# Performance work log

Hardware: AMD Instinct MI355X
Metric: run time of the kernel (lower is better)

## Reference

```python
import jax, jax.numpy as jnp
import numpy as np

N = 10000   # nodes
E = 320000  # edges
G = 64      # graphs in batch
D = 256     # gnn embedding dim
A = 118     # atomic_num_dim
OUT = 100   # spectrum dim
NUM_GINE = 2


def setup_inputs() -> dict:
    key = jax.random.key(0)
    ks = jax.random.split(key, 16)
    inp = {
        'atomic_num': jax.random.normal(ks[0], (N, A), dtype=jnp.float32),
        'length': jax.random.uniform(ks[1], (E,), dtype=jnp.float32),
        'src': jax.random.randint(ks[2], (E,), 0, N, dtype=jnp.int32),
        'dst': jax.random.randint(ks[3], (E,), 0, N, dtype=jnp.int32),
        'graph_ids': jnp.sort(jax.random.randint(ks[4], (N,), 0, G, dtype=jnp.int32)),
        # parameters
        'W_node': jax.random.normal(ks[5], (A, D), dtype=jnp.float32) / np.sqrt(A),
        'b_node': jnp.zeros((D,), dtype=jnp.float32),
        'W_edge': jax.random.normal(ks[6], (1, D), dtype=jnp.float32),
        'b_edge': jnp.zeros((D,), dtype=jnp.float32),
        'gine_eps': jnp.zeros((NUM_GINE,), dtype=jnp.float32),  # learnable eps per GINEConv
        'W_gnn': jax.random.normal(ks[7], (NUM_GINE, D, D), dtype=jnp.float32) / np.sqrt(D),
        'b_gnn': jnp.zeros((NUM_GINE, D), dtype=jnp.float32),
        'eps_param': jnp.array([1e-3], dtype=jnp.float32),  # unify_vector eps
        'W_mlp': jax.random.normal(ks[8], (D, OUT), dtype=jnp.float32) / np.sqrt(D),
        'b_mlp': jnp.zeros((OUT,), dtype=jnp.float32),
    }
    return inp


def reference(atomic_num, length, src, dst, graph_ids,
              W_node, b_node, W_edge, b_edge,
              gine_eps, W_gnn, b_gnn, eps_param, W_mlp, b_mlp):
    # node / edge embeddings
    h = atomic_num @ W_node + b_node            # [N, D]
    e = length[:, None] @ W_edge + b_edge       # [E, D]
    # GINEConv layers: m_ij = relu(h_src + e_ij); h_i' = W((1+eps)h_i + sum_j m_ij) + b
    for i in range(NUM_GINE):
        m = jax.nn.relu(h[src] + e)             # [E, D] gather + elementwise
        agg = jax.ops.segment_sum(m, dst, num_segments=N)  # scatter-sum to dst nodes
        h = ((1.0 + gine_eps[i]) * h + agg) @ W_gnn[i] + b_gnn[i]
    # sum_nodes pooling per graph
    feat = jax.ops.segment_sum(h, graph_ids, num_segments=G)  # [G, D]
    # unify_vector: global min/max normalization
    mn = jnp.min(feat)
    mx = jnp.max(feat)
    feat = (feat - mn) / (eps_param[0] + mx - mn)
    # MLP head (no hidden layers): Linear(D, 100)
    return feat @ W_mlp + b_mlp                 # [G, 100]
```

## Files before the change

kernel.cpp:

```cpp
#include <hip/hip_runtime.h>
#include <hip/hip_bf16.h>

#define N_NODES 10000
#define N_EDGES 320000
#define N_GRAPHS 64
#define DIM 256
#define ADIM 118
#define OUTD 100
#define CAP 96
#define CURPAD 16

typedef short bf8_t __attribute__((ext_vector_type(8)));
typedef float f4_t  __attribute__((ext_vector_type(4)));

__device__ __forceinline__ unsigned short f2bf(float f) {
    unsigned u = __float_as_uint(f);
    u += 0x7FFFu + ((u >> 16) & 1u);
    return (unsigned short)(u >> 16);
}
__device__ __forceinline__ float bf2f(unsigned short s) {
    return __uint_as_float(((unsigned)s) << 16);
}

__global__ __launch_bounds__(256) void convW_k(
    const float* __restrict__ Wn, const float* __restrict__ Wg,
    unsigned short* __restrict__ WnT, unsigned short* __restrict__ WgT,
    int* __restrict__ cursor, float* __restrict__ feat) {
    int i = blockIdx.x * 256 + threadIdx.x;
    if (i < 32768) {
        int c = i >> 7, k = i & 127;
        WnT[i] = (k < ADIM) ? f2bf(Wn[k * DIM + c]) : (unsigned short)0;
    } else {
        int j = i - 32768;
        int l = j >> 16, rem = j & 65535;
        int c = rem >> 8, k = rem & 255;
        WgT[j] = f2bf(Wg[l * 65536 + k * DIM + c]);
    }
    if (i < N_NODES * CURPAD) cursor[i] = (i >> 4) * CAP;
    if (i < N_GRAPHS * DIM) feat[i] = 0.f;
}

__global__ __launch_bounds__(256) void fill_k(
    const int* __restrict__ src, const int* __restrict__ dst,
    const float* __restrict__ len, int* __restrict__ cursor,
    int2* __restrict__ epack) {
    int j = blockIdx.x * 256 + threadIdx.x;
    if (j >= N_EDGES) return;
    int d = dst[j];
    int pos = atomicAdd(&cursor[d << 4], 1);
    if (pos < d * CAP + CAP)
        epack[pos] = make_int2(src[j], __float_as_int(len[j]));
}

#define AST 136
__global__ __launch_bounds__(256) void node_embed_k(
    const float* __restrict__ an, const unsigned short* __restrict__ WnT,
    const float* __restrict__ bn, unsigned short* __restrict__ hbf) {
    __shared__ __attribute__((aligned(16))) unsigned short xs[16 * AST];
    const int base = blockIdx.x * 16;
    const int tid = threadIdx.x;
    for (int i = tid; i < 16 * (AST - ADIM); i += 256) {
        int r = i / (AST - ADIM);
        int c = i - r * (AST - ADIM);
        xs[r * AST + ADIM + c] = 0;
    }
    for (int i = tid; i < 16 * 59; i += 256) {
        int r = i / 59;
        int c = (i - r * 59) * 2;
        float2 v = *(const float2*)(an + (size_t)(base + r) * ADIM + c);
        xs[r * AST + c]     = f2bf(v.x);
        xs[r * AST + c + 1] = f2bf(v.y);
    }
    __syncthreads();
    const int wave = tid >> 6, lane = tid & 63;
    const int m = lane & 15, quad = lane >> 4;
    bf8_t afrag[4];
    #pragma unroll
    for (int s = 0; s < 4; ++s)
        afrag[s] = *(const bf8_t*)&xs[m * AST + s * 32 + quad * 8];
    const int colbase = wave * 64;
    #pragma unroll
    for (int ct = 0; ct < 4; ++ct) {
        f4_t acc = (f4_t){0.f, 0.f, 0.f, 0.f};
        const unsigned short* wp = WnT + (size_t)(colbase + ct * 16 + m) * 128 + quad * 8;
        #pragma unroll
        for (int s = 0; s < 4; ++s) {
            bf8_t bfrag = *(const bf8_t*)(wp + s * 32);
            acc = __builtin_amdgcn_mfma_f32_16x16x32_bf16(afrag[s], bfrag, acc, 0, 0, 0);
        }
        int col = colbase + ct * 16 + m;
        float bb = bn[col];
        #pragma unroll
        for (int r = 0; r < 4; ++r)
            hbf[(size_t)(base + quad * 4 + r) * DIM + col] = f2bf(acc[r] + bb);
    }
}

__global__ __launch_bounds__(256) void gather_k(
    const unsigned short* __restrict__ hbf, const int* __restrict__ cursor,
    const int2* __restrict__ epack, const float* __restrict__ We,
    const float* __restrict__ be, const float* __restrict__ epsp, int layer,
    unsigned short* __restrict__ xbf) {
    const int B = blockIdx.x;
    const int half = (B >> 2) & 1;
    const int k = (B >> 3) * 4 + (B & 3);
    const int wave = threadIdx.x >> 6, lane = threadIdx.x & 63;
    const int node = __builtin_amdgcn_readfirstlane(k * 4 + wave);
    const int sub = lane >> 4;
    const int dp = half * 128 + (lane & 15) * 8;
    float4 wa = *(const float4*)(We + dp);
    float4 wc = *(const float4*)(We + dp + 4);
    float4 b0 = *(const float4*)(be + dp);
    float4 b1 = *(const float4*)(be + dp + 4);
    float w[8]  = {wa.x, wa.y, wa.z, wa.w, wc.x, wc.y, wc.z, wc.w};
    float bv[8] = {b0.x, b0.y, b0.z, b0.w, b1.x, b1.y, b1.z, b1.w};
    float acc[8];
    #pragma unroll
    for (int i = 0; i < 8; ++i) acc[i] = 0.f;
    const unsigned short* hb = hbf + dp;
    const int lo = node * CAP;
    const int cnt = min(__builtin_amdgcn_readfirstlane(cursor[node * CURPAD]) - lo, CAP);
    const int2* ep = epack + lo;
#define GATH(q) { \
    bf8_t a = *(const bf8_t*)(hb + (size_t)(q).x * DIM); \
    float l = __int_as_float((q).y); \
    _Pragma("unroll") \
    for (int d = 0; d < 8; ++d) \
        acc[d] += fmaxf(bf2f((unsigned short)a[d]) + fmaf(l, w[d], bv[d]), 0.f); }
    int t = 0;
    for (; t + 7 < cnt; t += 8) {
        int2 qa = ep[t + sub], qb = ep[t + 4 + sub];
        GATH(qa) GATH(qb)
    }
    for (; t + 3 < cnt; t += 4) {
        int2 q = ep[t + sub];
        GATH(q)
    }
    if (t < cnt && t + sub < cnt) {
        int2 q = ep[t + sub];
        GATH(q)
    }
#undef GATH
    #pragma unroll
    for (int d = 0; d < 8; ++d) {
        acc[d] += __shfl(acc[d], lane ^ 16, 64);
        acc[d] += __shfl(acc[d], lane ^ 32, 64);
    }
    if (sub == 0) {
        const float eps1 = 1.f + epsp[layer];
        bf8_t hv = *(const bf8_t*)(hbf + (size_t)node * DIM + dp);
        bf8_t o;
        #pragma unroll
        for (int d = 0; d < 8; ++d)
            o[d] = (short)f2bf(fmaf(eps1, bf2f((unsigned short)hv[d]), acc[d]));
        *(bf8_t*)(xbf + (size_t)node * DIM + dp) = o;
    }
}

#define XST 264
__global__ __launch_bounds__(256) void update_k(
    const unsigned short* __restrict__ xbf,
    const unsigned short* __restrict__ WT, const float* __restrict__ b,
    unsigned short* __restrict__ hout,
    const int* __restrict__ gid, float* __restrict__ feat, int do_pool) {
    __shared__ __attribute__((aligned(16))) unsigned short xs[16 * XST];
    __shared__ int gids[16];
    const int rb = blockIdx.x >> 1;
    const int halfc = blockIdx.x & 1;
    const int base = rb * 16;
    const int tid = threadIdx.x;
    #pragma unroll
    for (int cch = tid; cch < 512; cch += 256) {
        int rr = cch >> 5, k0 = (cch & 31) * 8;
        *(bf8_t*)&xs[rr * XST + k0] = *(const bf8_t*)(xbf + (size_t)(base + rr) * DIM + k0);
    }
    if (do_pool && tid < 16) gids[tid] = gid[base + tid];
    __syncthreads();
    const int wave = tid >> 6, lane = tid & 63;
    const int m = lane & 15, quad = lane >> 4;
    bf8_t afrag[8];
    #pragma unroll
    for (int s = 0; s < 8; ++s)
        afrag[s] = *(const bf8_t*)&xs[m * XST + s * 32 + quad * 8];
    const int colbase = halfc * 128 + wave * 32;
    #pragma unroll
    for (int ct = 0; ct < 2; ++ct) {
        const int col = colbase + ct * 16 + m;
        f4_t acc2 = (f4_t){0.f, 0.f, 0.f, 0.f};
        const unsigned short* wp = WT + (size_t)col * DIM + quad * 8;
        #pragma unroll
        for (int s = 0; s < 8; ++s) {
            bf8_t bfrag = *(const bf8_t*)(wp + s * 32);
            acc2 = __builtin_amdgcn_mfma_f32_16x16x32_bf16(afrag[s], bfrag, acc2, 0, 0, 0);
        }
        const float bb = b[col];
        if (!do_pool) {
            #pragma unroll
            for (int r = 0; r < 4; ++r)
                hout[(size_t)(base + quad * 4 + r) * DIM + col] = f2bf(acc2[r] + bb);
        } else {
            if (gids[0] == gids[15]) {
                float v = acc2[0] + acc2[1] + acc2[2] + acc2[3] + 4.f * bb;
                v += __shfl(v, lane ^ 16, 64);
                v += __shfl(v, lane ^ 32, 64);
                if (quad == 0) atomicAdd(&feat[(size_t)gids[0] * DIM + col], v);
            } else {
                float run = 0.f;
                int cur = gids[quad * 4];
                #pragma unroll
                for (int r = 0; r < 4; ++r) {
                    int g = gids[quad * 4 + r];
                    if (g != cur) {
                        atomicAdd(&feat[(size_t)cur * DIM + col], run);
                        run = 0.f;
                        cur = g;
                    }
                    run += acc2[r] + bb;
                }
                atomicAdd(&feat[(size_t)cur * DIM + col], run);
            }
        }
    }
}

__global__ __launch_bounds__(256) void headmm_k(
    const float* __restrict__ feat, const float* __restrict__ Wm,
    const float* __restrict__ bm, const float* __restrict__ epsp,
    float* __restrict__ out) {
    __shared__ float frow[DIM];
    __shared__ float smn[4], smx[4], sMn, sMx;
    const int g = blockIdx.x;
    const int tid = threadIdx.x;
    float mn = 3.4e38f, mx = -3.4e38f;
    for (int i = tid; i < N_GRAPHS * DIM; i += 256) {
        float v = feat[i];
        mn = fminf(mn, v);
        mx = fmaxf(mx, v);
    }
    frow[tid] = feat[g * DIM + tid];
    #pragma unroll
    for (int off = 32; off > 0; off >>= 1) {
        mn = fminf(mn, __shfl_down(mn, off, 64));
        mx = fmaxf(mx, __shfl_down(mx, off, 64));
    }
    const int wave = tid >> 6, lane = tid & 63;
    if (lane == 0) { smn[wave] = mn; smx[wave] = mx; }
    __syncthreads();
    if (tid == 0) {
        sMn = fminf(fminf(smn[0], smn[1]), fminf(smn[2], smn[3]));
        sMx = fmaxf(fmaxf(smx[0], smx[1]), fmaxf(smx[2], smx[3]));
    }
    __syncthreads();
    if (tid < OUTD) {
        const float mnv = sMn;
        const float inv = 1.f / (epsp[0] + sMx - mnv);
        float acc = 0.f;
        for (int d = 0; d < DIM; ++d)
            acc += (frow[d] - mnv) * Wm[d * OUTD + tid];
        out[g * OUTD + tid] = acc * inv + bm[tid];
    }
}

extern "C" void kernel_launch(void* const* d_in, const int* in_sizes, int n_in,
                              void* d_out, int out_size, void* d_ws, size_t ws_size,
                              hipStream_t stream) {
    const float* atomic_num = (const float*)d_in[0];
    const float* length     = (const float*)d_in[1];
    const int*   src        = (const int*)d_in[2];
    const int*   dst        = (const int*)d_in[3];
    const int*   gid        = (const int*)d_in[4];
    const float* W_node     = (const float*)d_in[5];
    const float* b_node     = (const float*)d_in[6];
    const float* W_edge     = (const float*)d_in[7];
    const float* b_edge     = (const float*)d_in[8];
    const float* gine_eps   = (const float*)d_in[9];
    const float* W_gnn      = (const float*)d_in[10];
    const float* b_gnn      = (const float*)d_in[11];
    const float* eps_param  = (const float*)d_in[12];
    const float* W_mlp      = (const float*)d_in[13];
    const float* b_mlp      = (const float*)d_in[14];
    float* out = (float*)d_out;

    float* feat = (float*)d_ws;
    int* cursor = (int*)(feat + (size_t)N_GRAPHS * DIM);
    int2* epack = (int2*)(cursor + (size_t)N_NODES * CURPAD + 16);
    unsigned short* hbf0 = (unsigned short*)(epack + (size_t)N_NODES * CAP);
    unsigned short* hbf1 = hbf0 + (size_t)N_NODES * DIM;
    unsigned short* xbf  = hbf1 + (size_t)N_NODES * DIM;
    unsigned short* WnT  = xbf + (size_t)N_NODES * DIM;
    unsigned short* WgT  = WnT + 256 * 128;

    convW_k<<<640, 256, 0, stream>>>(W_node, W_gnn, WnT, WgT, cursor, feat);
    fill_k<<<N_EDGES / 256, 256, 0, stream>>>(src, dst, length, cursor, epack);
    node_embed_k<<<N_NODES / 16, 256, 0, stream>>>(atomic_num, WnT, b_node, hbf0);

    gather_k<<<5000, 256, 0, stream>>>(
        hbf0, cursor, epack, W_edge, b_edge, gine_eps, 0, xbf);
    update_k<<<(N_NODES / 16) * 2, 256, 0, stream>>>(
        xbf, WgT, b_gnn, hbf1, gid, feat, 0);
    gather_k<<<5000, 256, 0, stream>>>(
        hbf1, cursor, epack, W_edge, b_edge, gine_eps, 1, xbf);
    update_k<<<(N_NODES / 16) * 2, 256, 0, stream>>>(
        xbf, WgT + 256 * 256, b_gnn + DIM, hbf0, gid, feat, 1);

    headmm_k<<<N_GRAPHS, 256, 0, stream>>>(feat, W_mlp, b_mlp, eps_param, out);
}
```

Measured before the change: 205.5 us.

## Fold edge bias into node features, use packed FMA in gather, merge setup kernels

```diff
diff --git a/kernel.cpp b/kernel.cpp
--- a/kernel.cpp
+++ b/kernel.cpp
@@ -12,6 +12,7 @@
 
 typedef short bf8_t __attribute__((ext_vector_type(8)));
 typedef float f4_t  __attribute__((ext_vector_type(4)));
+typedef float f2_t  __attribute__((ext_vector_type(2)));
 
 __device__ __forceinline__ unsigned short f2bf(float f) {
     unsigned u = __float_as_uint(f);
@@ -21,41 +22,50 @@
 __device__ __forceinline__ float bf2f(unsigned short s) {
     return __uint_as_float(((unsigned)s) << 16);
 }
-
-__global__ __launch_bounds__(256) void convW_k(
+__device__ __forceinline__ f2_t pk_fma(f2_t a, f2_t b, f2_t c) {
+    f2_t d;
+    asm("v_pk_fma_f32 %0, %1, %2, %3" : "=v"(d) : "v"(a), "v"(b), "v"(c));
+    return d;
+}
+__device__ __forceinline__ f2_t pk_add(f2_t a, f2_t b) {
+    f2_t d;
+    asm("v_pk_add_f32 %0, %1, %2" : "=v"(d) : "v"(a), "v"(b));
+    return d;
+}
+
+__global__ __launch_bounds__(256) void setup_k(
+    const int* __restrict__ src, const int* __restrict__ dst,
+    const float* __restrict__ len,
     const float* __restrict__ Wn, const float* __restrict__ Wg,
     unsigned short* __restrict__ WnT, unsigned short* __restrict__ WgT,
-    int* __restrict__ cursor, float* __restrict__ feat) {
-    int i = blockIdx.x * 256 + threadIdx.x;
-    if (i < 32768) {
-        int c = i >> 7, k = i & 127;
-        WnT[i] = (k < ADIM) ? f2bf(Wn[k * DIM + c]) : (unsigned short)0;
+    int* __restrict__ cnt, int2* __restrict__ epack) {
+    const int B = blockIdx.x;
+    const int tid = threadIdx.x;
+    if (B < 1250) {
+        int j = B * 256 + tid;
+        int d = dst[j];
+        int pos = atomicAdd(&cnt[d << 4], 1);
+        if (pos < CAP)
+            epack[d * CAP + pos] = make_int2(src[j] * DIM, __float_as_int(len[j]));
     } else {
-        int j = i - 32768;
-        int l = j >> 16, rem = j & 65535;
-        int c = rem >> 8, k = rem & 255;
-        WgT[j] = f2bf(Wg[l * 65536 + k * DIM + c]);
-    }
-    if (i < N_NODES * CURPAD) cursor[i] = (i >> 4) * CAP;
-    if (i < N_GRAPHS * DIM) feat[i] = 0.f;
-}
-
-__global__ __launch_bounds__(256) void fill_k(
-    const int* __restrict__ src, const int* __restrict__ dst,
-    const float* __restrict__ len, int* __restrict__ cursor,
-    int2* __restrict__ epack) {
-    int j = blockIdx.x * 256 + threadIdx.x;
-    if (j >= N_EDGES) return;
-    int d = dst[j];
-    int pos = atomicAdd(&cursor[d << 4], 1);
-    if (pos < d * CAP + CAP)
-        epack[pos] = make_int2(src[j], __float_as_int(len[j]));
+        int i = (B - 1250) * 256 + tid;
+        if (i < 32768) {
+            int c = i >> 7, k = i & 127;
+            WnT[i] = (k < ADIM) ? f2bf(Wn[k * DIM + c]) : (unsigned short)0;
+        } else {
+            int j = i - 32768;
+            int l = j >> 16, rem = j & 65535;
+            int c = rem >> 8, k = rem & 255;
+            WgT[j] = f2bf(Wg[l * 65536 + k * DIM + c]);
+        }
+    }
 }
 
 #define AST 136
 __global__ __launch_bounds__(256) void node_embed_k(
     const float* __restrict__ an, const unsigned short* __restrict__ WnT,
-    const float* __restrict__ bn, unsigned short* __restrict__ hbf) {
+    const float* __restrict__ bn, const float* __restrict__ be,
+    unsigned short* __restrict__ hbf) {
     __shared__ __attribute__((aligned(16))) unsigned short xs[16 * AST];
     const int base = blockIdx.x * 16;
     const int tid = threadIdx.x;
@@ -89,7 +99,7 @@
             acc = __builtin_amdgcn_mfma_f32_16x16x32_bf16(afrag[s], bfrag, acc, 0, 0, 0);
         }
         int col = colbase + ct * 16 + m;
-        float bb = bn[col];
+        float bb = bn[col] + be[col];
         #pragma unroll
         for (int r = 0; r < 4; ++r)
             hbf[(size_t)(base + quad * 4 + r) * DIM + col] = f2bf(acc[r] + bb);
@@ -97,7 +107,7 @@
 }
 
 __global__ __launch_bounds__(256) void gather_k(
-    const unsigned short* __restrict__ hbf, const int* __restrict__ cursor,
+    const unsigned short* __restrict__ hbf, const int* __restrict__ cnt,
     const int2* __restrict__ epack, const float* __restrict__ We,
     const float* __restrict__ be, const float* __restrict__ epsp, int layer,
     unsigned short* __restrict__ xbf) {
@@ -110,49 +120,70 @@
     const int dp = half * 128 + (lane & 15) * 8;
     float4 wa = *(const float4*)(We + dp);
     float4 wc = *(const float4*)(We + dp + 4);
-    float4 b0 = *(const float4*)(be + dp);
-    float4 b1 = *(const float4*)(be + dp + 4);
-    float w[8]  = {wa.x, wa.y, wa.z, wa.w, wc.x, wc.y, wc.z, wc.w};
-    float bv[8] = {b0.x, b0.y, b0.z, b0.w, b1.x, b1.y, b1.z, b1.w};
-    float acc[8];
-    #pragma unroll
-    for (int i = 0; i < 8; ++i) acc[i] = 0.f;
+    f2_t ww[4];
+    ww[0] = (f2_t){wa.x, wa.y}; ww[1] = (f2_t){wa.z, wa.w};
+    ww[2] = (f2_t){wc.x, wc.y}; ww[3] = (f2_t){wc.z, wc.w};
+    const float eps1 = 1.f + epsp[layer];
+    float4 ba = *(const float4*)(be + dp);
+    float4 bc = *(const float4*)(be + dp + 4);
+    f2_t ebe[4];
+    ebe[0] = (f2_t){eps1 * ba.x, eps1 * ba.y};
+    ebe[1] = (f2_t){eps1 * ba.z, eps1 * ba.w};
+    ebe[2] = (f2_t){eps1 * bc.x, eps1 * bc.y};
+    ebe[3] = (f2_t){eps1 * bc.z, eps1 * bc.w};
+    f2_t acc2[4];
+    #pragma unroll
+    for (int i = 0; i < 4; ++i) acc2[i] = (f2_t){0.f, 0.f};
     const unsigned short* hb = hbf + dp;
-    const int lo = node * CAP;
-    const int cnt = min(__builtin_amdgcn_readfirstlane(cursor[node * CURPAD]) - lo, CAP);
-    const int2* ep = epack + lo;
+    const int ce = min(__builtin_amdgcn_readfirstlane(cnt[node << 4]), CAP);
+    const int2* ep = epack + node * CAP;
 #define GATH(q) { \
-    bf8_t a = *(const bf8_t*)(hb + (size_t)(q).x * DIM); \
-    float l = __int_as_float((q).y); \
+    const uint4 ar = *(const uint4*)(hb + (unsigned)(q).x); \
+    const float l = __int_as_float((q).y); \
+    f2_t lpk; lpk.x = l; lpk.y = l; \
     _Pragma("unroll") \
-    for (int d = 0; d < 8; ++d) \
-        acc[d] += fmaxf(bf2f((unsigned short)a[d]) + fmaf(l, w[d], bv[d]), 0.f); }
+    for (int p = 0; p < 4; ++p) { \
+        unsigned u = (&ar.x)[p]; \
+        f2_t h; \
+        h.x = __uint_as_float(u << 16); \
+        h.y = __uint_as_float(u & 0xffff0000u); \
+        f2_t mm = pk_fma(lpk, ww[p], h); \
+        mm.x = fmaxf(mm.x, 0.f); \
+        mm.y = fmaxf(mm.y, 0.f); \
+        acc2[p] = pk_add(acc2[p], mm); \
+    } }
     int t = 0;
-    for (; t + 7 < cnt; t += 8) {
+    for (; t + 7 < ce; t += 8) {
         int2 qa = ep[t + sub], qb = ep[t + 4 + sub];
         GATH(qa) GATH(qb)
     }
-    for (; t + 3 < cnt; t += 4) {
+    for (; t + 3 < ce; t += 4) {
         int2 q = ep[t + sub];
         GATH(q)
     }
-    if (t < cnt && t + sub < cnt) {
+    if (t < ce && t + sub < ce) {
         int2 q = ep[t + sub];
         GATH(q)
     }
 #undef GATH
     #pragma unroll
-    for (int d = 0; d < 8; ++d) {
-        acc[d] += __shfl(acc[d], lane ^ 16, 64);
-        acc[d] += __shfl(acc[d], lane ^ 32, 64);
+    for (int p = 0; p < 4; ++p) {
+        acc2[p].x += __shfl(acc2[p].x, lane ^ 16, 64);
+        acc2[p].y += __shfl(acc2[p].y, lane ^ 16, 64);
+        acc2[p].x += __shfl(acc2[p].x, lane ^ 32, 64);
+        acc2[p].y += __shfl(acc2[p].y, lane ^ 32, 64);
     }
     if (sub == 0) {
-        const float eps1 = 1.f + epsp[layer];
-        bf8_t hv = *(const bf8_t*)(hbf + (size_t)node * DIM + dp);
+        const uint4 hr = *(const uint4*)(hbf + (size_t)node * DIM + dp);
         bf8_t o;
         #pragma unroll
-        for (int d = 0; d < 8; ++d)
-            o[d] = (short)f2bf(fmaf(eps1, bf2f((unsigned short)hv[d]), acc[d]));
+        for (int p = 0; p < 4; ++p) {
+            unsigned u = (&hr.x)[p];
+            float hlo = __uint_as_float(u << 16);
+            float hhi = __uint_as_float(u & 0xffff0000u);
+            o[2 * p]     = (short)f2bf(fmaf(eps1, hlo, acc2[p].x - ebe[p].x));
+            o[2 * p + 1] = (short)f2bf(fmaf(eps1, hhi, acc2[p].y - ebe[p].y));
+        }
         *(bf8_t*)(xbf + (size_t)node * DIM + dp) = o;
     }
 }
@@ -161,7 +192,7 @@
 __global__ __launch_bounds__(256) void update_k(
     const unsigned short* __restrict__ xbf,
     const unsigned short* __restrict__ WT, const float* __restrict__ b,
-    unsigned short* __restrict__ hout,
+    const float* __restrict__ be, unsigned short* __restrict__ hout,
     const int* __restrict__ gid, float* __restrict__ feat, int do_pool) {
     __shared__ __attribute__((aligned(16))) unsigned short xs[16 * XST];
     __shared__ int gids[16];
@@ -193,12 +224,13 @@
             bf8_t bfrag = *(const bf8_t*)(wp + s * 32);
             acc2 = __builtin_amdgcn_mfma_f32_16x16x32_bf16(afrag[s], bfrag, acc2, 0, 0, 0);
         }
-        const float bb = b[col];
         if (!do_pool) {
+            const float bb = b[col] + be[col];
             #pragma unroll
             for (int r = 0; r < 4; ++r)
                 hout[(size_t)(base + quad * 4 + r) * DIM + col] = f2bf(acc2[r] + bb);
         } else {
+            const float bb = b[col];
             if (gids[0] == gids[15]) {
                 float v = acc2[0] + acc2[1] + acc2[2] + acc2[3] + 4.f * bb;
                 v += __shfl(v, lane ^ 16, 64);
@@ -282,26 +314,30 @@
     float* out = (float*)d_out;
 
     float* feat = (float*)d_ws;
-    int* cursor = (int*)(feat + (size_t)N_GRAPHS * DIM);
-    int2* epack = (int2*)(cursor + (size_t)N_NODES * CURPAD + 16);
+    int* cnt    = (int*)(feat + (size_t)N_GRAPHS * DIM);
+    int2* epack = (int2*)(cnt + (size_t)N_NODES * CURPAD);
     unsigned short* hbf0 = (unsigned short*)(epack + (size_t)N_NODES * CAP);
     unsigned short* hbf1 = hbf0 + (size_t)N_NODES * DIM;
     unsigned short* xbf  = hbf1 + (size_t)N_NODES * DIM;
     unsigned short* WnT  = xbf + (size_t)N_NODES * DIM;
     unsigned short* WgT  = WnT + 256 * 128;
 
-    convW_k<<<640, 256, 0, stream>>>(W_node, W_gnn, WnT, WgT, cursor, feat);
-    fill_k<<<N_EDGES / 256, 256, 0, stream>>>(src, dst, length, cursor, epack);
-    node_embed_k<<<N_NODES / 16, 256, 0, stream>>>(atomic_num, WnT, b_node, hbf0);
+    hipMemsetAsync(d_ws, 0,
+                   (size_t)N_GRAPHS * DIM * 4 + (size_t)N_NODES * CURPAD * 4,
+                   stream);
+    setup_k<<<1250 + 640, 256, 0, stream>>>(
+        src, dst, length, W_node, W_gnn, WnT, WgT, cnt, epack);
+    node_embed_k<<<N_NODES / 16, 256, 0, stream>>>(
+        atomic_num, WnT, b_node, b_edge, hbf0);
 
     gather_k<<<5000, 256, 0, stream>>>(
-        hbf0, cursor, epack, W_edge, b_edge, gine_eps, 0, xbf);
+        hbf0, cnt, epack, W_edge, b_edge, gine_eps, 0, xbf);
     update_k<<<(N_NODES / 16) * 2, 256, 0, stream>>>(
-        xbf, WgT, b_gnn, hbf1, gid, feat, 0);
+        xbf, WgT, b_gnn, b_edge, hbf1, gid, feat, 0);
     gather_k<<<5000, 256, 0, stream>>>(
-        hbf1, cursor, epack, W_edge, b_edge, gine_eps, 1, xbf);
+        hbf1, cnt, epack, W_edge, b_edge, gine_eps, 1, xbf);
     update_k<<<(N_NODES / 16) * 2, 256, 0, stream>>>(
-        xbf, WgT + 256 * 256, b_gnn + DIM, hbf0, gid, feat, 1);
+        xbf, WgT + 256 * 256, b_gnn + DIM, b_edge, hbf0, gid, feat, 1);
 
     headmm_k<<<N_GRAPHS, 256, 0, stream>>>(feat, W_mlp, b_mlp, eps_param, out);
 }
```

After: 203.9 us. Within noise of the previous version (-0.8%).
